# Performance work log

Measured on AMD Instinct MI355X. Metric: run time of the kernel, lower is better.

The kernel has to match this reference:

```python
import jax, jax.numpy as jnp
import numpy as np
import math

INV = 1.0 / (2.0 * math.pi) ** 2  # 1/(2*pi)^2 normalization used throughout
EPS = 1e-8


def setup_inputs() -> dict:
    key = jax.random.key(0)
    ks = jax.random.split(key, 5)
    N, K, J = 512, 8, 6
    return {
        "x_hat": jax.random.normal(ks[0], (N, N, 2), jnp.float32),
        "phi_hat_real": jax.random.normal(ks[1], (N, N), jnp.float32),
        "phi_hat_imag": jax.random.normal(ks[2], (N, N), jnp.float32),
        "psi_hat_real": jax.random.normal(ks[3], (K, J, N, N), jnp.float32),
        "psi_hat_imag": jax.random.normal(ks[4], (K, J, N, N), jnp.float32),
    }


def reference(x_hat, phi_hat_real, phi_hat_imag, psi_hat_real, psi_hat_imag):
    K, J, N, _ = psi_hat_real.shape
    NN = N * N
    phi2 = phi_hat_real ** 2 + phi_hat_imag ** 2  # [N,N]

    # zeroth-order coefficient: full spatial mean of |x_hat|^2 * |phi_hat|^2
    s0 = INV * jnp.mean((x_hat[:, :, 0] ** 2 + x_hat[:, :, 1] ** 2) * phi2)

    # first layer: complex multiply in Fourier domain, ifft2, modulus, fft2
    xc = jax.lax.complex(x_hat[:, :, 0], x_hat[:, :, 1])          # [N,N] complex
    psic = jax.lax.complex(psi_hat_real, psi_hat_imag)            # [K,J,N,N] complex
    temp = jnp.fft.ifft2(xc[None, None] * psic, axes=(-2, -1))    # [K,J,N,N] complex
    mod = jnp.sqrt(temp.real ** 2 + temp.imag ** 2 + EPS)         # modulus nonlinearity
    t2 = jnp.fft.fft2(mod, axes=(-2, -1))                         # rfft onesided=False == full fft of real
    power = (t2.real ** 2 + t2.imag ** 2).reshape(K, J, NN)       # |U1_hat|^2

    # first-order coefficients a[k,i] = INV * mean(power * phi2)
    a = INV * (power @ phi2.reshape(NN)) / NN                     # [K,J]

    # second-order coefficients via GEMM over spatial dim:
    # B[k,i,m,j] = INV * mean_xy(power[k,i] * |psi[m,j]|^2)
    psi2 = (psi_hat_real ** 2 + psi_hat_imag ** 2).reshape(K, J, NN)
    B = INV * jnp.einsum('kin,mjn->kimj', power, psi2) / NN       # [K,J,K,J]

    # assemble output in the same concatenation order as the torch loop:
    # [s0, a_0, b_0(flattened over k,m,j'), a_1, b_1, ..., a_{J-1}]
    pieces = [s0[None]]
    for i in range(J):
        pieces.append(a[:, i])
        if i < J - 1:
            pieces.append(B[:, i, :, i + 1:J].reshape(-1))
    return jnp.concatenate(pieces, axis=0)
```

## Files before the change

kernel.cpp:

```cpp
#include <hip/hip_runtime.h>
#include <hip/hip_fp16.h>

#define Nn 512
#define NNe 262144
#define CST 546
#define SST 521

__device__ __forceinline__ float2 f2(float x, float y){ return make_float2(x, y); }
__device__ __forceinline__ float2 cadd(float2 a, float2 b){ return f2(a.x+b.x, a.y+b.y); }
__device__ __forceinline__ float2 csub(float2 a, float2 b){ return f2(a.x-b.x, a.y-b.y); }
__device__ __forceinline__ float2 cmul(float2 a, float2 b){
    return f2(a.x*b.x - a.y*b.y, a.x*b.y + a.y*b.x);
}
__device__ __forceinline__ int pidx(int p){ return p + (p>>4) + (p>>7); }
#define WFENCE() __builtin_amdgcn_wave_barrier()

template<int SGN>
__device__ __forceinline__ void fft8(float2 a[8]){
    const float r = 0.7071067811865476f;
    const float S = (float)SGN;
    float2 u0 = cadd(a[0], a[4]), u1 = cadd(a[1], a[5]);
    float2 u2 = cadd(a[2], a[6]), u3 = cadd(a[3], a[7]);
    float2 v0 = csub(a[0], a[4]), v1 = csub(a[1], a[5]);
    float2 v2 = csub(a[2], a[6]), v3 = csub(a[3], a[7]);
    v1 = cmul(v1, f2(r, S*r));
    v2 = cmul(v2, f2(0.f, S));
    v3 = cmul(v3, f2(-r, S*r));
    float2 p0 = cadd(u0, u2), p1 = cadd(u1, u3);
    float2 q0 = csub(u0, u2), q1 = cmul(csub(u1, u3), f2(0.f, S));
    a[0] = cadd(p0, p1); a[4] = csub(p0, p1);
    a[2] = cadd(q0, q1); a[6] = csub(q0, q1);
    p0 = cadd(v0, v2); p1 = cadd(v1, v3);
    q0 = csub(v0, v2); q1 = cmul(csub(v1, v3), f2(0.f, S));
    a[1] = cadd(p0, p1); a[5] = csub(p0, p1);
    a[3] = cadd(q0, q1); a[7] = csub(q0, q1);
}

__device__ __forceinline__ float2 twdp(int idx, float inv){
    float ang = 6.283185307179586f * (inv * (float)idx);
    float s, c;
    __sincosf(ang, &s, &c);
    return f2(c, s);
}

template<int SGN>
__device__ void fft512_dif_i(float2 v[8], float2* buf, int lane){
    fft8<SGN>(v);
    {
        float2 w1 = twdp(lane, 1.f/512.f);
        if (SGN < 0) w1.y = -w1.y;
        float2 w  = f2(1.f, 0.f);
        #pragma unroll
        for (int r = 0; r < 8; ++r){
            buf[pidx(r*64 + lane)] = cmul(v[r], w);
            w = cmul(w, w1);
        }
    }
    WFENCE();
    int rb = (lane >> 3) * 64, t2 = lane & 7;
    float2 y[8];
    #pragma unroll
    for (int q = 0; q < 8; ++q) y[q] = buf[pidx(rb + t2 + 8*q)];
    fft8<SGN>(y);
    WFENCE();
    {
        float2 w2 = twdp(t2, 1.f/64.f);
        if (SGN < 0) w2.y = -w2.y;
        float2 w  = f2(1.f, 0.f);
        #pragma unroll
        for (int r = 0; r < 8; ++r){
            buf[pidx(rb + r*8 + t2)] = cmul(y[r], w);
            w = cmul(w, w2);
        }
    }
    WFENCE();
    int base = rb + t2*8;
    #pragma unroll
    for (int q = 0; q < 8; ++q) v[q] = buf[pidx(base + q)];
    fft8<SGN>(v);
}

template<int SGN>
__device__ void fft512_dit_i(float2 v[8], float2* buf, int lane){
    int rb = (lane >> 3) * 64, t2 = lane & 7;
    fft8<SGN>(v);
    int base = rb + t2*8;
    #pragma unroll
    for (int q = 0; q < 8; ++q) buf[pidx(base + q)] = v[q];
    WFENCE();
    float2 y[8];
    #pragma unroll
    for (int r = 0; r < 8; ++r) y[r] = buf[pidx(rb + r*8 + t2)];
    {
        float2 w2 = twdp(t2, 1.f/64.f);
        if (SGN < 0) w2.y = -w2.y;
        float2 w  = f2(1.f, 0.f);
        #pragma unroll
        for (int r = 0; r < 8; ++r){
            y[r] = cmul(y[r], w);
            w = cmul(w, w2);
        }
    }
    fft8<SGN>(y);
    WFENCE();
    #pragma unroll
    for (int q = 0; q < 8; ++q) buf[pidx(rb + t2 + 8*q)] = y[q];
    WFENCE();
    #pragma unroll
    for (int r = 0; r < 8; ++r) v[r] = buf[pidx(r*64 + lane)];
    {
        float2 w1 = twdp(lane, 1.f/512.f);
        if (SGN < 0) w1.y = -w1.y;
        float2 w  = f2(1.f, 0.f);
        #pragma unroll
        for (int r = 0; r < 8; ++r){
            v[r] = cmul(v[r], w);
            w = cmul(w, w1);
        }
    }
    fft8<SGN>(v);
}

__global__ __launch_bounds__(256, 6)
void k_mulrow(const float2* __restrict__ xh, const float* __restrict__ pr,
              const float* __restrict__ pi, __half2* __restrict__ temp,
              __half* __restrict__ psi2h){
    __shared__ float2 lds[4][548];
    int wave = threadIdx.x >> 6, lane = threadIdx.x & 63;
    int img  = blockIdx.x >> 7;
    int row  = ((blockIdx.x & 127) << 2) | wave;
    size_t boff = (size_t)img * NNe + (size_t)row * Nn;
    const float2* xr = xh + (size_t)row * Nn;
    float2 v[8];
    #pragma unroll
    for (int q = 0; q < 8; ++q){
        int x = lane + 64*q;
        float2 xv = xr[x];
        float2 pv = f2(pr[boff + x], pi[boff + x]);
        psi2h[boff + x] = __float2half_rn(pv.x*pv.x + pv.y*pv.y);
        v[q] = cmul(xv, pv);
    }
    fft512_dif_i<1>(v, lds[wave], lane);
    __half2* outp = temp + boff;
    #pragma unroll
    for (int q = 0; q < 8; ++q) outp[64*q + lane] = __floats2half2_rn(v[q].x, v[q].y);
}

__global__ __launch_bounds__(512, 3)
void k_colfused(__half2* __restrict__ temp){
    __shared__ __align__(16) unsigned char smem[8 * CST * 8];
    __half2* st = (__half2*)smem;
    int img = blockIdx.x >> 5;
    int x0  = (blockIdx.x & 31) << 4;
    __half2* src = temp + (size_t)img * NNe + x0;
    for (int i = threadIdx.x; i < 2048; i += 512){
        int row = i >> 2, c4 = (i & 3) << 2;
        uint4 u = *(const uint4*)&src[(size_t)row * Nn + c4];
        st[(c4+0)*SST + row] = *(__half2*)&u.x;
        st[(c4+1)*SST + row] = *(__half2*)&u.y;
        st[(c4+2)*SST + row] = *(__half2*)&u.z;
        st[(c4+3)*SST + row] = *(__half2*)&u.w;
    }
    __syncthreads();
    int wave = threadIdx.x >> 6, lane = threadIdx.x & 63;
    int c0 = 2*wave, c1 = c0 + 1;
    float2 a[8], b[8];
    #pragma unroll
    for (int q = 0; q < 8; ++q) a[q] = __half22float2(st[c0*SST + lane + 64*q]);
    #pragma unroll
    for (int q = 0; q < 8; ++q) b[q] = __half22float2(st[c1*SST + lane + 64*q]);
    __syncthreads();
    float2* buf = (float2*)smem + wave * CST;
    const float sc = 3.814697265625e-06f;
    fft512_dif_i<1>(a, buf, lane);
    WFENCE();
    fft512_dif_i<1>(b, buf, lane);
    float2 z[8];
    #pragma unroll
    for (int q = 0; q < 8; ++q){
        float r0 = a[q].x*sc, i0 = a[q].y*sc;
        float r1 = b[q].x*sc, i1 = b[q].y*sc;
        z[q] = f2(sqrtf(r0*r0 + i0*i0 + 1e-8f), sqrtf(r1*r1 + i1*i1 + 1e-8f));
    }
    WFENCE();
    fft512_dit_i<-1>(z, buf, lane);
    #pragma unroll
    for (int q = 0; q < 8; ++q) buf[pidx(lane + 64*q)] = z[q];
    WFENCE();
    float2 zr[8];
    #pragma unroll
    for (int q = 0; q < 8; ++q) zr[q] = buf[pidx((512 - (lane + 64*q)) & 511)];
    __half2 m0[8], m1[8];
    #pragma unroll
    for (int q = 0; q < 8; ++q){
        float2 zv = z[q], w = zr[q];
        m0[q] = __floats2half2_rn(0.5f*(zv.x + w.x), 0.5f*(zv.y - w.y));
        m1[q] = __floats2half2_rn(0.5f*(zv.y + w.y), 0.5f*(w.x - zv.x));
    }
    __syncthreads();
    #pragma unroll
    for (int q = 0; q < 8; ++q){
        st[c0*SST + lane + 64*q] = m0[q];
        st[c1*SST + lane + 64*q] = m1[q];
    }
    __syncthreads();
    for (int i = threadIdx.x; i < 2048; i += 512){
        int row = i >> 2, c4 = (i & 3) << 2;
        uint4 u;
        *(__half2*)&u.x = st[(c4+0)*SST + row];
        *(__half2*)&u.y = st[(c4+1)*SST + row];
        *(__half2*)&u.z = st[(c4+2)*SST + row];
        *(__half2*)&u.w = st[(c4+3)*SST + row];
        *(uint4*)&src[(size_t)row * Nn + c4] = u;
    }
}

__global__ __launch_bounds__(256, 6)
void k_rowpow(const __half2* __restrict__ temp, __half* __restrict__ powerh){
    __shared__ float2 lds[4][548];
    int wave = threadIdx.x >> 6, lane = threadIdx.x & 63;
    int img  = blockIdx.x >> 7;
    int row  = ((blockIdx.x & 127) << 2) | wave;
    const __half2* src = temp + (size_t)img * NNe + (size_t)row * Nn;
    float2 v[8];
    #pragma unroll
    for (int q = 0; q < 8; ++q) v[q] = __half22float2(src[64*q + lane]);
    fft512_dit_i<-1>(v, lds[wave], lane);
    __half* dst = powerh + (size_t)img * NNe + (size_t)row * Nn;
    #pragma unroll
    for (int q = 0; q < 8; ++q)
        dst[lane + 64*q] = __float2half_rn((v[q].x*v[q].x + v[q].y*v[q].y) * 0.00390625f);
}

__global__ __launch_bounds__(256)
void k_s0(const float2* __restrict__ xh, const float* __restrict__ phr,
          const float* __restrict__ phii, float* __restrict__ part){
    int gid = blockIdx.x*256 + threadIdx.x;
    float acc = 0.f;
    for (int n = gid; n < NNe; n += 256*256){
        float2 x = xh[n];
        float a = phr[n], b = phii[n];
        acc += (x.x*x.x + x.y*x.y) * (a*a + b*b);
    }
    #pragma unroll
    for (int o = 32; o > 0; o >>= 1) acc += __shfl_down(acc, o, 64);
    __shared__ float wsum[4];
    int wave = threadIdx.x >> 6, lane = threadIdx.x & 63;
    if (lane == 0) wsum[wave] = acc;
    __syncthreads();
    if (threadIdx.x == 0) part[blockIdx.x] = wsum[0]+wsum[1]+wsum[2]+wsum[3];
}

__global__ __launch_bounds__(128)
void k_gemm(const __half* __restrict__ powerh, const __half* __restrict__ psi2h,
            const float* __restrict__ phr, const float* __restrict__ phii,
            float* __restrict__ partC){
    __shared__ __align__(16) float P[2][48][68];
    __shared__ __align__(16) float W[2][56][68];
    int wave = threadIdx.x >> 6, lane = threadIdx.x & 63;
    float (*Pw)[68] = P[wave];
    float (*Ww)[68] = W[wave];
    int gw = blockIdx.x*2 + wave;
    int lm = lane >> 3, lw = lane & 7;
    float acc[6][7] = {};
    #pragma unroll
    for (int r = 49; r < 56; ++r){
        Ww[r][lane] = 0.f;
        if (lane < 4) Ww[r][64 + lane] = 0.f;
    }
    int n0 = gw * 256;
    for (int st = 0; st < 4; ++st){
        int nb = n0 + st*64;
        WFENCE();
        #pragma unroll
        for (int rr = 0; rr < 12; ++rr){
            int row = rr*4 + (lane >> 4);
            int c4  = (lane & 15) * 4;
            size_t off = (size_t)row*NNe + nb + c4;
            const __half2* p2 = (const __half2*)&powerh[off];
            float2 f0 = __half22float2(p2[0]);
            float2 f1 = __half22float2(p2[1]);
            *(float4*)&Pw[row][c4] = make_float4(f0.x, f0.y, f1.x, f1.y);
        }
        #pragma unroll
        for (int rr = 0; rr < 12; ++rr){
            int row = rr*4 + (lane >> 4);
            int c4  = (lane & 15) * 4;
            size_t off = (size_t)row*NNe + nb + c4;
            const __half2* p2 = (const __half2*)&psi2h[off];
            float2 f0 = __half22float2(p2[0]);
            float2 f1 = __half22float2(p2[1]);
            *(float4*)&Ww[row][c4] = make_float4(f0.x, f0.y, f1.x, f1.y);
        }
        if (lane < 16){
            int c4 = lane * 4;
            float4 a = *(const float4*)&phr[nb + c4];
            float4 b = *(const float4*)&phii[nb + c4];
            float4 w4;
            w4.x = a.x*a.x + b.x*b.x; w4.y = a.y*a.y + b.y*b.y;
            w4.z = a.z*a.z + b.z*b.z; w4.w = a.w*a.w + b.w*b.w;
            *(float4*)&Ww[48][c4] = w4;
        }
        WFENCE();
        #pragma unroll 2
        for (int nn = 0; nn < 64; nn += 4){
            float4 pa[6], wb[7];
            #pragma unroll
            for (int i = 0; i < 6; ++i) pa[i] = *(const float4*)&Pw[lm + 8*i][nn];
            #pragma unroll
            for (int j = 0; j < 7; ++j) wb[j] = *(const float4*)&Ww[lw + 8*j][nn];
            #pragma unroll
            for (int i = 0; i < 6; ++i)
                #pragma unroll
                for (int j = 0; j < 7; ++j){
                    float s = acc[i][j];
                    s = fmaf(pa[i].x, wb[j].x, s);
                    s = fmaf(pa[i].y, wb[j].y, s);
                    s = fmaf(pa[i].z, wb[j].z, s);
                    s = fmaf(pa[i].w, wb[j].w, s);
                    acc[i][j] = s;
                }
        }
    }
    float* outp = partC + (size_t)gw * 2400;
    #pragma unroll
    for (int i = 0; i < 6; ++i)
        #pragma unroll
        for (int j = 0; j < 7; ++j){
            int m = lm + 8*i, wc = lw + 8*j;
            if (wc < 49) outp[m*50 + wc] = acc[i][j];
        }
}

__global__ __launch_bounds__(256)
void k_redc1(const float* __restrict__ partC, float* __restrict__ partC2){
    __shared__ float red[4][64];
    int es = threadIdx.x & 63, wave = threadIdx.x >> 6;
    int e = blockIdx.x*64 + es;
    int b0 = blockIdx.y*64 + wave*16;
    float s = 0.f;
    if (e < 2400){
        #pragma unroll
        for (int u = 0; u < 16; ++u) s += partC[(size_t)(b0+u)*2400 + e];
    }
    red[wave][es] = s;
    __syncthreads();
    if (wave == 0 && e < 2400)
        partC2[(size_t)blockIdx.y*2400 + e] = red[0][es]+red[1][es]+red[2][es]+red[3][es];
}

__global__ __launch_bounds__(256)
void k_final(const float* __restrict__ partC2, const float* __restrict__ partS0,
             float* __restrict__ outp, float SC0, float SCC){
    __shared__ float CFs[2400];
    __shared__ float ssum[4];
    int tid = threadIdx.x, wave = tid >> 6, lane = tid & 63;
    for (int e = tid; e < 2400; e += 256){
        float s = 0.f;
        #pragma unroll
        for (int u = 0; u < 16; ++u) s += partC2[(size_t)u*2400 + e];
        CFs[e] = SCC * s;
    }
    float a = partS0[tid];
    #pragma unroll
    for (int o = 32; o > 0; o >>= 1) a += __shfl_down(a, o, 64);
    if (lane == 0) ssum[wave] = a;
    __syncthreads();
    if (tid == 0) outp[0] = SC0 * (ssum[0]+ssum[1]+ssum[2]+ssum[3]);
    int off = 1;
    for (int i = 0; i < 6; ++i){
        if (tid < 8) outp[off + tid] = CFs[(tid*6 + i)*50 + 48];
        off += 8;
        if (i < 5){
            int nj = 5 - i, cnt = 64 * nj;
            for (int p = tid; p < cnt; p += 256){
                int j2 = p % nj;
                int km = p / nj;
                int m = km & 7, k = km >> 3;
                outp[off + p] = CFs[(k*6 + i)*50 + m*6 + (i + 1 + j2)];
            }
            off += cnt;
        }
    }
}

extern "C" void kernel_launch(void* const* d_in, const int* in_sizes, int n_in,
                              void* d_out, int out_size, void* d_ws, size_t ws_size,
                              hipStream_t stream){
    (void)in_sizes; (void)n_in; (void)out_size; (void)ws_size;
    const float2* xh  = (const float2*)d_in[0];
    const float*  phr = (const float*)d_in[1];
    const float*  phi_= (const float*)d_in[2];
    const float*  psr = (const float*)d_in[3];
    const float*  psi_= (const float*)d_in[4];
    float* outp = (float*)d_out;
    float* ws   = (float*)d_ws;

    size_t o_power = 0;
    size_t o_partC = o_power + (size_t)24 * NNe;
    size_t o_pC2   = o_partC + (size_t)1024 * 2400;
    size_t o_s0    = o_pC2 + (size_t)16 * 2400;
    size_t o_temp  = o_s0 + 256;
    size_t o_psi2  = o_temp + (size_t)48 * NNe;
    __half*  powerh= (__half*)(ws + o_power);
    float*   partC = ws + o_partC;
    float*   partC2= ws + o_pC2;
    float*   ps0   = ws + o_s0;
    __half2* temp  = (__half2*)(ws + o_temp);
    __half*  psi2h = (__half*)(ws + o_psi2);

    const double INVd = 1.0 / (4.0 * 3.14159265358979323846 * 3.14159265358979323846);
    const float SC0 = (float)(INVd / (double)NNe);
    const float SCC = (float)(INVd / (double)NNe * 256.0);

    k_s0<<<dim3(256), dim3(256), 0, stream>>>(xh, phr, phi_, ps0);
    k_mulrow<<<dim3(48*128), dim3(256), 0, stream>>>(xh, psr, psi_, temp, psi2h);
    k_colfused<<<dim3(48*32), dim3(512), 0, stream>>>(temp);
    k_rowpow<<<dim3(48*128), dim3(256), 0, stream>>>(temp, powerh);
    k_gemm<<<dim3(512), dim3(128), 0, stream>>>(powerh, psi2h, phr, phi_, partC);
    k_redc1<<<dim3(38, 16), dim3(256), 0, stream>>>(partC, partC2);
    k_final<<<dim3(1), dim3(256), 0, stream>>>(partC2, ps0, outp, SC0, SCC);
}
```

Before: 141.5 us.

## Drop two-for-one real FFT packing in column kernel, one wave per column

```diff
diff --git a/kernel.cpp b/kernel.cpp
--- a/kernel.cpp
+++ b/kernel.cpp
@@ -146,14 +146,16 @@
     for (int q = 0; q < 8; ++q) outp[64*q + lane] = __floats2half2_rn(v[q].x, v[q].y);
 }
 
-__global__ __launch_bounds__(512, 3)
+__global__ __launch_bounds__(1024, 8)
 void k_colfused(__half2* __restrict__ temp){
-    __shared__ __align__(16) unsigned char smem[8 * CST * 8];
+    __shared__ __align__(16) unsigned char smem[16 * CST * 8];
     __half2* st = (__half2*)smem;
     int img = blockIdx.x >> 5;
     int x0  = (blockIdx.x & 31) << 4;
     __half2* src = temp + (size_t)img * NNe + x0;
-    for (int i = threadIdx.x; i < 2048; i += 512){
+    #pragma unroll
+    for (int it = 0; it < 2; ++it){
+        int i = it*1024 + threadIdx.x;
         int row = i >> 2, c4 = (i & 3) << 2;
         uint4 u = *(const uint4*)&src[(size_t)row * Nn + c4];
         st[(c4+0)*SST + row] = *(__half2*)&u.x;
@@ -163,48 +165,30 @@
     }
     __syncthreads();
     int wave = threadIdx.x >> 6, lane = threadIdx.x & 63;
-    int c0 = 2*wave, c1 = c0 + 1;
-    float2 a[8], b[8];
-    #pragma unroll
-    for (int q = 0; q < 8; ++q) a[q] = __half22float2(st[c0*SST + lane + 64*q]);
-    #pragma unroll
-    for (int q = 0; q < 8; ++q) b[q] = __half22float2(st[c1*SST + lane + 64*q]);
+    float2 v[8];
+    #pragma unroll
+    for (int q = 0; q < 8; ++q) v[q] = __half22float2(st[wave*SST + lane + 64*q]);
     __syncthreads();
     float2* buf = (float2*)smem + wave * CST;
     const float sc = 3.814697265625e-06f;
-    fft512_dif_i<1>(a, buf, lane);
-    WFENCE();
-    fft512_dif_i<1>(b, buf, lane);
-    float2 z[8];
+    fft512_dif_i<1>(v, buf, lane);
     #pragma unroll
     for (int q = 0; q < 8; ++q){
-        float r0 = a[q].x*sc, i0 = a[q].y*sc;
-        float r1 = b[q].x*sc, i1 = b[q].y*sc;
-        z[q] = f2(sqrtf(r0*r0 + i0*i0 + 1e-8f), sqrtf(r1*r1 + i1*i1 + 1e-8f));
-    }
-    WFENCE();
-    fft512_dit_i<-1>(z, buf, lane);
-    #pragma unroll
-    for (int q = 0; q < 8; ++q) buf[pidx(lane + 64*q)] = z[q];
-    WFENCE();
-    float2 zr[8];
-    #pragma unroll
-    for (int q = 0; q < 8; ++q) zr[q] = buf[pidx((512 - (lane + 64*q)) & 511)];
-    __half2 m0[8], m1[8];
-    #pragma unroll
-    for (int q = 0; q < 8; ++q){
-        float2 zv = z[q], w = zr[q];
-        m0[q] = __floats2half2_rn(0.5f*(zv.x + w.x), 0.5f*(zv.y - w.y));
-        m1[q] = __floats2half2_rn(0.5f*(zv.y + w.y), 0.5f*(w.x - zv.x));
-    }
-    __syncthreads();
-    #pragma unroll
-    for (int q = 0; q < 8; ++q){
-        st[c0*SST + lane + 64*q] = m0[q];
-        st[c1*SST + lane + 64*q] = m1[q];
-    }
-    __syncthreads();
-    for (int i = threadIdx.x; i < 2048; i += 512){
+        float re = v[q].x * sc, im = v[q].y * sc;
+        v[q] = f2(sqrtf(re*re + im*im + 1e-8f), 0.f);
+    }
+    WFENCE();
+    fft512_dit_i<-1>(v, buf, lane);
+    __half2 m[8];
+    #pragma unroll
+    for (int q = 0; q < 8; ++q) m[q] = __floats2half2_rn(v[q].x, v[q].y);
+    __syncthreads();
+    #pragma unroll
+    for (int q = 0; q < 8; ++q) st[wave*SST + lane + 64*q] = m[q];
+    __syncthreads();
+    #pragma unroll
+    for (int it = 0; it < 2; ++it){
+        int i = it*1024 + threadIdx.x;
         int row = i >> 2, c4 = (i & 3) << 2;
         uint4 u;
         *(__half2*)&u.x = st[(c4+0)*SST + row];
@@ -415,7 +399,7 @@
 
     k_s0<<<dim3(256), dim3(256), 0, stream>>>(xh, phr, phi_, ps0);
     k_mulrow<<<dim3(48*128), dim3(256), 0, stream>>>(xh, psr, psi_, temp, psi2h);
-    k_colfused<<<dim3(48*32), dim3(512), 0, stream>>>(temp);
+    k_colfused<<<dim3(48*32), dim3(1024), 0, stream>>>(temp);
     k_rowpow<<<dim3(48*128), dim3(256), 0, stream>>>(temp, powerh);
     k_gemm<<<dim3(512), dim3(128), 0, stream>>>(powerh, psi2h, phr, phi_, partC);
     k_redc1<<<dim3(38, 16), dim3(256), 0, stream>>>(partC, partC2);
```

Measured after the change: 143.1 us. About the same (+1.2%).
